# Optimization experiments

Measured on AMD Instinct MI355X. Metric: run time of the kernel, lower is better.

## Reference

```python
import jax, jax.numpy as jnp
import numpy as np

B, S, D = 2, 4096, 512   # batch, seq_len, input_dim
W, H = 256, 4            # memory width (d_model), attention heads
DH = W // H              # per-head depth


def _dense(x, w, b):
    return x @ w + b


def setup_inputs() -> dict:
    key = jax.random.key(0)
    ks = jax.random.split(key, 24)
    def w(k, shape):
        return jax.random.normal(k, shape, dtype=jnp.float32) * 0.02
    inp = {
        "x": jax.random.normal(ks[0], (B, S, D), dtype=jnp.float32),
        # outer q/k/v projections D -> W
        "qp_w": w(ks[1], (D, W)), "qp_b": jnp.zeros((W,), jnp.float32),
        "kp_w": w(ks[2], (D, W)), "kp_b": jnp.zeros((W,), jnp.float32),
        "vp_w": w(ks[3], (D, W)), "vp_b": jnp.zeros((W,), jnp.float32),
        # MHA internal projections W -> W
        "wq_w": w(ks[4], (W, W)), "wq_b": jnp.zeros((W,), jnp.float32),
        "wk_w": w(ks[5], (W, W)), "wk_b": jnp.zeros((W,), jnp.float32),
        "wv_w": w(ks[6], (W, W)), "wv_b": jnp.zeros((W,), jnp.float32),
        "wo_w": w(ks[7], (W, W)), "wo_b": jnp.zeros((W,), jnp.float32),
        # deep MLP memory (depth=2, gelu) + its output proj W -> W
        "m0_w": w(ks[8], (W, W)), "m0_b": jnp.zeros((W,), jnp.float32),
        "m1_w": w(ks[9], (W, W)), "m1_b": jnp.zeros((W,), jnp.float32),
        "mo_w": w(ks[10], (W, W)), "mo_b": jnp.zeros((W,), jnp.float32),
        # final output projection W -> D
        "op_w": w(ks[11], (W, D)), "op_b": jnp.zeros((D,), jnp.float32),
    }
    return inp


def reference(x, qp_w, qp_b, kp_w, kp_b, vp_w, vp_b,
              wq_w, wq_b, wk_w, wk_b, wv_w, wv_b, wo_w, wo_b,
              m0_w, m0_b, m1_w, m1_b, mo_w, mo_b, op_w, op_b):
    # outer projections (D -> W)
    q0 = _dense(x, qp_w, qp_b)
    k0 = _dense(x, kp_w, kp_b)
    v0 = _dense(x, vp_w, vp_b)
    # MHA internal projections (W -> W)
    q = _dense(q0, wq_w, wq_b)
    k = _dense(k0, wk_w, wk_b)
    v = _dense(v0, wv_w, wv_b)
    # split heads: [B,S,W] -> [B,H,S,DH]
    def split(t):
        return t.reshape(B, S, H, DH).transpose(0, 2, 1, 3)
    qh, kh, vh = split(q), split(k), split(v)
    scores = jnp.einsum('bhqd,bhkd->bhqk', qh, kh) / jnp.sqrt(jnp.float32(DH))
    attn = jax.nn.softmax(scores, axis=-1)
    ctx = jnp.einsum('bhqk,bhkd->bhqd', attn, vh)
    ctx = ctx.transpose(0, 2, 1, 3).reshape(B, S, W)
    retrieved = _dense(ctx, wo_w, wo_b)
    # deep MLP memory (exact gelu, matching keras 'gelu')
    h = jax.nn.gelu(_dense(retrieved, m0_w, m0_b), approximate=False)
    h = jax.nn.gelu(_dense(h, m1_w, m1_b), approximate=False)
    mem = _dense(h, mo_w, mo_b)
    # final projection + residual
    out = _dense(mem, op_w, op_b) + x
    return out
```

## Files before the change

### kernel.cpp

```cpp
#include <hip/hip_runtime.h>
#include <cstdint>
#include <cstddef>


#define GAS(p) ((const __attribute__((address_space(1))) void*)(p))
#define LAS(p) ((__attribute__((address_space(3))) void*)(p))

typedef __attribute__((ext_vector_type(8))) short bfrag;
typedef __attribute__((ext_vector_type(4))) float facc;
typedef uint16_t u16;

__device__ __forceinline__ u16 f2bf(float f) {
  uint32_t u = __float_as_uint(f);
  u += 0x7fffu + ((u >> 16) & 1u);
  return (u16)(u >> 16);
}
__device__ __forceinline__ float bf2f(u16 h) {
  return __uint_as_float((uint32_t)h << 16);
}
__device__ __forceinline__ float gelu_exact(float v) {
  return 0.5f * v * (1.f + erff(v * 0.70710678118654752440f));
}
__device__ __forceinline__ facc mfma16(bfrag a, bfrag b, facc c) {
  return __builtin_amdgcn_mfma_f32_16x16x32_bf16(a, b, c, 0, 0, 0);
}

__device__ __forceinline__ bfrag lds_frag(const u16* lds, int row, int kk, int ln) {
  int kb  = (kk << 6) + ((ln >> 4) << 4);
  int off = (row << 7) + (kb ^ ((row & 7) << 4));
  return *(const bfrag*)((const char*)lds + off);
}

template <int ROWS>
__device__ __forceinline__ void stage_tile(const u16* gbase, int ldK, u16* lds,
                                           int wv, int ln) {
#pragma unroll
  for (int i = 0; i < ROWS / 32; i++) {
    int seg = (i << 2) + wv;
    int row = (seg << 3) + (ln >> 3);
    int kb  = (ln & 7) << 4;
    const char* g = (const char*)(gbase + (size_t)row * ldK) +
                    (kb ^ ((row & 7) << 4));
    __builtin_amdgcn_global_load_lds(GAS(g), LAS(lds + (seg << 9)), 16, 0, 0);
  }
}

template <int EPI, int BN>
__global__ __launch_bounds__(256) void gemm_bt(
    const u16* __restrict__ A, const u16* __restrict__ Bt,
    const float* __restrict__ bias, const float* __restrict__ resid,
    u16* __restrict__ obf, float* __restrict__ of32,
    u16* __restrict__ qb, u16* __restrict__ kb2, u16* __restrict__ vb,
    int M, int N, int K, int zsA, int zsB, int zRows) {
  const int t = threadIdx.x, wv = t >> 6, ln = t & 63;
  const int wr = wv >> 1, wc = wv & 1;
  const int m0 = blockIdx.y << 7, n0 = blockIdx.x * BN;
  const int z = blockIdx.z;
  A  += (size_t)z * zsA;
  Bt += (size_t)z * zsB;
  constexpr int NJ = BN / 32;

  __shared__ __align__(16) u16 Al[128 * 64];
  __shared__ __align__(16) u16 Bl[BN * 64];

  facc acc[4][NJ];
#pragma unroll
  for (int i = 0; i < 4; i++)
#pragma unroll
    for (int j = 0; j < NJ; j++)
#pragma unroll
      for (int r = 0; r < 4; r++) acc[i][j][r] = 0.f;

  const u16* Ab = A + (size_t)m0 * K;
  const u16* Bb = Bt + (size_t)n0 * K;
  stage_tile<128>(Ab, K, Al, wv, ln);
  stage_tile<BN>(Bb, K, Bl, wv, ln);

  const int nk = K >> 6;
  for (int kt = 0; kt < nk; ++kt) {
    __syncthreads();
#pragma unroll
    for (int kk = 0; kk < 2; kk++) {
      bfrag av[4], bv[NJ];
#pragma unroll
      for (int i = 0; i < 4; i++)
        av[i] = lds_frag(Al, (wr << 6) + (i << 4) + (ln & 15), kk, ln);
#pragma unroll
      for (int j = 0; j < NJ; j++)
        bv[j] = lds_frag(Bl, wc * (BN / 2) + (j << 4) + (ln & 15), kk, ln);
#pragma unroll
      for (int i = 0; i < 4; i++)
#pragma unroll
        for (int j = 0; j < NJ; j++)
          acc[i][j] = mfma16(av[i], bv[j], acc[i][j]);
    }
    if (kt + 1 < nk) {
      __syncthreads();
      stage_tile<128>(Ab + (kt + 1) * 64, K, Al, wv, ln);
      stage_tile<BN>(Bb + (kt + 1) * 64, K, Bl, wv, ln);
    }
  }

  const int rb = (ln >> 4) << 2, cb = ln & 15;
#pragma unroll
  for (int i = 0; i < 4; i++) {
#pragma unroll
    for (int j = 0; j < NJ; j++) {
      const int col = n0 + wc * (BN / 2) + (j << 4) + cb;
      const float bcol = bias ? bias[col] : 0.f;
#pragma unroll
      for (int r = 0; r < 4; r++) {
        const int row = m0 + (wr << 6) + (i << 4) + rb + r;
        float val = acc[i][j][r] + bcol;
        if (EPI == 0) {
          obf[(size_t)(z * zRows + row) * N + col] = f2bf(val);
        } else if (EPI == 1) {
          obf[(size_t)row * N + col] = f2bf(gelu_exact(val));
        } else if (EPI == 2) {
          const int sec = col >> 8, cc = col & 255, h = cc >> 6, dh = cc & 63;
          const int b = row >> 12, s = row & 4095;
          const size_t idx = (((size_t)(b * 4 + h)) * 4096 + s) * 64 + dh;
          const u16 bvv = f2bf(val);
          if (sec == 0) qb[idx] = bvv;
          else if (sec == 1) kb2[idx] = bvv;
          else vb[idx] = bvv;
        } else {
          of32[(size_t)row * N + col] = val + resid[(size_t)row * N + col];
        }
      }
    }
  }
}

__global__ __launch_bounds__(256) void attn2(
    const u16* __restrict__ qg, const u16* __restrict__ kg,
    const u16* __restrict__ vtg, u16* __restrict__ Opart,
    float* __restrict__ lpart) {
  const int t = threadIdx.x, wv = t >> 6, ln = t & 63;
  const int lo = ln & 15, hi = ln >> 4;
  const int qt = blockIdx.x, bh = blockIdx.y, half = blockIdx.z;
  const int qbase = qt * 128 + wv * 32;
  const u16* Q  = qg + ((size_t)bh * 4096 + qbase) * 64;
  const u16* Kb = kg + ((size_t)bh * 4096 + half * 2048) * 64;
  const u16* Vt = vtg + (size_t)bh * 64 * 4096 + half * 2048;

  __shared__ __align__(16) u16 Klds[2][4096];
  __shared__ __align__(16) u16 Vlds[2][4096];
  __shared__ __align__(16) u16 Plds[4][2048];
  u16* Pw = Plds[wv];

  bfrag qf[2][2];
#pragma unroll
  for (int g = 0; g < 2; g++) {
    const u16* qp = Q + (((g << 4) + lo) << 6) + (hi << 3);
    qf[g][0] = *(const bfrag*)qp;
    qf[g][1] = *(const bfrag*)(qp + 32);
  }
  facc oacc[2][4];
#pragma unroll
  for (int g = 0; g < 2; g++)
#pragma unroll
    for (int nb = 0; nb < 4; nb++)
#pragma unroll
      for (int r = 0; r < 4; r++) oacc[g][nb][r] = 0.f;
  float l_acc[2] = {0.f, 0.f};

  stage_tile<64>(Kb, 64, Klds[0], wv, ln);
  stage_tile<64>(Vt, 4096, Vlds[0], wv, ln);

  for (int kt = 0; kt < 32; ++kt) {
    const int cur = kt & 1;
    __syncthreads();
    if (kt < 31) {
      stage_tile<64>(Kb + (size_t)(kt + 1) * 64 * 64, 64, Klds[cur ^ 1], wv, ln);
      stage_tile<64>(Vt + (kt + 1) * 64, 4096, Vlds[cur ^ 1], wv, ln);
    }
    facc sa[2][4];
#pragma unroll
    for (int g = 0; g < 2; g++)
#pragma unroll
      for (int kb = 0; kb < 4; kb++)
#pragma unroll
        for (int r = 0; r < 4; r++) sa[g][kb][r] = 0.f;
#pragma unroll
    for (int kb = 0; kb < 4; kb++) {
      bfrag a0 = lds_frag(Klds[cur], (kb << 4) + lo, 0, ln);
      bfrag a1 = lds_frag(Klds[cur], (kb << 4) + lo, 1, ln);
      sa[0][kb] = mfma16(a0, qf[0][0], sa[0][kb]);
      sa[0][kb] = mfma16(a1, qf[0][1], sa[0][kb]);
      sa[1][kb] = mfma16(a0, qf[1][0], sa[1][kb]);
      sa[1][kb] = mfma16(a1, qf[1][1], sa[1][kb]);
    }
#pragma unroll
    for (int g = 0; g < 2; g++) {
      const int row = (g << 4) + lo;
      char* pb = (char*)Pw + (row << 7);
      const int sw = (row & 7) << 4;
      float ls = 0.f;
#pragma unroll
      for (int kb = 0; kb < 4; kb++) {
        float p0 = exp2f(sa[g][kb][0] * 0.18033688011112042f);
        float p1 = exp2f(sa[g][kb][1] * 0.18033688011112042f);
        float p2 = exp2f(sa[g][kb][2] * 0.18033688011112042f);
        float p3 = exp2f(sa[g][kb][3] * 0.18033688011112042f);
        ls += (p0 + p1) + (p2 + p3);
        uint32_t w0, w1;
        asm("v_cvt_pk_bf16_f32 %0, %1, %2" : "=v"(w0) : "v"(p0), "v"(p1));
        asm("v_cvt_pk_bf16_f32 %0, %1, %2" : "=v"(w1) : "v"(p2), "v"(p3));
        uint2 w2;
        w2.x = w0; w2.y = w1;
        *(uint2*)(pb + (((kb << 5) + (hi << 3)) ^ sw)) = w2;
      }
      l_acc[g] += ls;
    }
#pragma unroll
    for (int c = 0; c < 2; c++) {
      bfrag pa0 = lds_frag(Pw, lo, c, ln);
      bfrag pa1 = lds_frag(Pw, 16 + lo, c, ln);
#pragma unroll
      for (int nb = 0; nb < 4; nb++) {
        bfrag vf = lds_frag(Vlds[cur], (nb << 4) + lo, c, ln);
        oacc[0][nb] = mfma16(pa0, vf, oacc[0][nb]);
        oacc[1][nb] = mfma16(pa1, vf, oacc[1][nb]);
      }
    }
  }

#pragma unroll
  for (int g = 0; g < 2; g++) {
    l_acc[g] += __shfl_xor(l_acc[g], 16);
    l_acc[g] += __shfl_xor(l_acc[g], 32);
  }
  const size_t obase = (size_t)(half * 8 + bh) * 4096;
#pragma unroll
  for (int g = 0; g < 2; g++) {
#pragma unroll
    for (int nb = 0; nb < 4; nb++)
#pragma unroll
      for (int r = 0; r < 4; r++) {
        const int q = qbase + (g << 4) + (hi << 2) + r;
        Opart[(obase + q) * 64 + (nb << 4) + lo] = f2bf(oacc[g][nb][r]);
      }
    if (hi == 0) lpart[obase + qbase + (g << 4) + lo] = l_acc[g];
  }
}

__global__ __launch_bounds__(256) void attn_combine(
    const u16* __restrict__ Opart, const float* __restrict__ lpart,
    u16* __restrict__ ctx) {
  const int idx = blockIdx.x * 256 + threadIdx.x;
  const int d0 = (idx & 7) << 3, s = (idx >> 3) & 4095, bh = idx >> 15;
  const size_t o0 = ((size_t)bh * 4096 + s) * 64 + d0;
  const size_t o1 = o0 + (size_t)8 * 4096 * 64;
  bfrag a = *(const bfrag*)(Opart + o0);
  bfrag b = *(const bfrag*)(Opart + o1);
  const float rl = 1.f / (lpart[bh * 4096 + s] + lpart[32768 + bh * 4096 + s]);
  bfrag o;
#pragma unroll
  for (int j = 0; j < 8; j++)
    o[j] = (short)f2bf((bf2f((u16)a[j]) + bf2f((u16)b[j])) * rl);
  *(bfrag*)(ctx + ((size_t)(bh >> 2) * 4096 + s) * 256 + ((bh & 3) << 6) + d0) = o;
}

__global__ __launch_bounds__(256) void conv_bf16(const float* __restrict__ x,
                                                 u16* __restrict__ xb) {
  const size_t i = ((size_t)blockIdx.x * 256 + threadIdx.x) * 8;
  float4 a = *(const float4*)(x + i);
  float4 b = *(const float4*)(x + i + 4);
  bfrag o;
  o[0] = (short)f2bf(a.x); o[1] = (short)f2bf(a.y);
  o[2] = (short)f2bf(a.z); o[3] = (short)f2bf(a.w);
  o[4] = (short)f2bf(b.x); o[5] = (short)f2bf(b.y);
  o[6] = (short)f2bf(b.z); o[7] = (short)f2bf(b.w);
  *(bfrag*)(xb + i) = o;
}

__global__ __launch_bounds__(256) void conv_weights(
    const float* __restrict__ qp, const float* __restrict__ kp,
    const float* __restrict__ vp, const float* __restrict__ mo,
    u16* __restrict__ owqkv, u16* __restrict__ mo_bf) {
  const int i = (blockIdx.x * 256 + threadIdx.x) * 4;
  const float* s; u16* dst; int off;
  if (i < 131072)      { s = qp; dst = owqkv;          off = i; }
  else if (i < 262144) { s = kp; dst = owqkv + 131072; off = i - 131072; }
  else if (i < 393216) { s = vp; dst = owqkv + 262144; off = i - 262144; }
  else                 { s = mo; dst = mo_bf;          off = i - 393216; }
  float4 v = *(const float4*)(s + off);
  ushort4 o;
  o.x = f2bf(v.x); o.y = f2bf(v.y); o.z = f2bf(v.z); o.w = f2bf(v.w);
  *(ushort4*)(dst + off) = o;
}

__global__ __launch_bounds__(256) void transp_w6(
    const float* wo, const float* m0, const float* m1,
    const float* wq, const float* wk, const float* wv,
    u16* wo_t, u16* m0_t, u16* m1_t, u16* wqT, u16* wkT, u16* wvT) {
  const int mi = blockIdx.x >> 8, n = blockIdx.x & 255, k = threadIdx.x;
  const float* s; u16* d;
  switch (mi) {
    case 0: s = wo; d = wo_t; break;
    case 1: s = m0; d = m0_t; break;
    case 2: s = m1; d = m1_t; break;
    case 3: s = wq; d = wqT; break;
    case 4: s = wk; d = wkT; break;
    default: s = wv; d = wvT; break;
  }
  d[(size_t)n * 256 + k] = f2bf(s[(size_t)k * 256 + n]);
}

__global__ __launch_bounds__(256) void transp_op(const float* __restrict__ op_w,
                                                 u16* __restrict__ opT) {
  const int d = blockIdx.x, c = threadIdx.x;
  opT[(size_t)d * 256 + c] = f2bf(op_w[(size_t)c * 512 + d]);
}

__global__ __launch_bounds__(256) void fuse_bias(
    const float* qp_b, const float* kp_b, const float* vp_b,
    const float* wq_w, const float* wk_w, const float* wv_w,
    const float* wq_b, const float* wk_b, const float* wv_b,
    const float* mo_b, const float* op_w, const float* op_b,
    float* bqkv, float* bmo) {
  const int z = blockIdx.x, t = threadIdx.x;
  __shared__ float red[4];
  float v;
  if (z < 768) {
    const int sec = z >> 8, nn = z & 255;
    const float* ob = sec == 0 ? qp_b : (sec == 1 ? kp_b : vp_b);
    const float* iw = sec == 0 ? wq_w : (sec == 1 ? wk_w : wv_w);
    v = ob[t] * iw[(size_t)t * 256 + nn];
  } else {
    v = mo_b[t] * op_w[(size_t)t * 512 + (z - 768)];
  }
#pragma unroll
  for (int o = 32; o > 0; o >>= 1) v += __shfl_down(v, o);
  if ((t & 63) == 0) red[t >> 6] = v;
  __syncthreads();
  if (t == 0) {
    float s = red[0] + red[1] + red[2] + red[3];
    if (z < 768) {
      const int sec = z >> 8, nn = z & 255;
      const float* ib = sec == 0 ? wq_b : (sec == 1 ? wk_b : wv_b);
      bqkv[z] = s + ib[nn];
    } else {
      bmo[z - 768] = s + op_b[z - 768];
    }
  }
}

__global__ __launch_bounds__(256) void transpose_v(const u16* __restrict__ v,
                                                   u16* __restrict__ vt) {
  const int bh = blockIdx.x >> 6, st = blockIdx.x & 63, t = threadIdx.x;
  __shared__ u16 tile[64][65];
  const u16* src = v + ((size_t)bh * 4096 + st * 64) * 64;
  {
    const int r = t >> 2, c0 = (t & 3) << 4;
    bfrag x0 = *(const bfrag*)(src + (size_t)r * 64 + c0);
    bfrag x1 = *(const bfrag*)(src + (size_t)r * 64 + c0 + 8);
#pragma unroll
    for (int j = 0; j < 8; j++) {
      tile[r][c0 + j] = (u16)x0[j];
      tile[r][c0 + 8 + j] = (u16)x1[j];
    }
  }
  __syncthreads();
  {
    const int d = t >> 2, s0 = (t & 3) << 4;
    bfrag y0, y1;
#pragma unroll
    for (int j = 0; j < 8; j++) {
      y0[j] = (short)tile[s0 + j][d];
      y1[j] = (short)tile[s0 + 8 + j][d];
    }
    u16* dst = vt + ((size_t)bh * 64 + d) * 4096 + (st << 6) + s0;
    *(bfrag*)(dst) = y0;
    *(bfrag*)(dst + 8) = y1;
  }
}

extern "C" void kernel_launch(void* const* d_in, const int* in_sizes, int n_in,
                              void* d_out, int out_size, void* d_ws,
                              size_t ws_size, hipStream_t stream) {
  const float* x    = (const float*)d_in[0];
  const float* qp_w = (const float*)d_in[1];
  const float* qp_b = (const float*)d_in[2];
  const float* kp_w = (const float*)d_in[3];
  const float* kp_b = (const float*)d_in[4];
  const float* vp_w = (const float*)d_in[5];
  const float* vp_b = (const float*)d_in[6];
  const float* wq_w = (const float*)d_in[7];
  const float* wq_b = (const float*)d_in[8];
  const float* wk_w = (const float*)d_in[9];
  const float* wk_b = (const float*)d_in[10];
  const float* wv_w = (const float*)d_in[11];
  const float* wv_b = (const float*)d_in[12];
  const float* wo_w = (const float*)d_in[13];
  const float* wo_b = (const float*)d_in[14];
  const float* m0_w = (const float*)d_in[15];
  const float* m0_b = (const float*)d_in[16];
  const float* m1_w = (const float*)d_in[17];
  const float* m1_b = (const float*)d_in[18];
  const float* mo_w = (const float*)d_in[19];
  const float* mo_b = (const float*)d_in[20];
  const float* op_w = (const float*)d_in[21];
  const float* op_b = (const float*)d_in[22];
  float* out = (float*)d_out;

  char* ws = (char*)d_ws;
  u16*   xb     = (u16*)(ws);
  u16*   q_buf  = (u16*)(ws + 8388608);
  u16*   k_buf  = (u16*)(ws + 12582912);
  u16*   v_buf  = (u16*)(ws + 16777216);
  u16*   vt_buf = (u16*)(ws + 20971520);
  u16*   ctx    = (u16*)(ws + 25165824);
  u16*   Opart  = (u16*)(ws + 29360128);
  float* lpart  = (float*)(ws + 37748736);
  u16*   Wqkv_t = (u16*)(ws + 38010880);
  u16*   owqkv  = (u16*)(ws + 38797312);
  u16*   wqkvT  = (u16*)(ws + 39583744);
  u16*   wo_t   = (u16*)(ws + 39976960);
  u16*   m0_t   = (u16*)(ws + 40108032);
  u16*   m1_t   = (u16*)(ws + 40239104);
  u16*   opT    = (u16*)(ws + 40370176);
  u16*   mo_bf  = (u16*)(ws + 40632320);
  u16*   Wmo_t  = (u16*)(ws + 40763392);
  float* bqkv   = (float*)(ws + 41025536);
  float* bmo    = (float*)(ws + 41029632);
  u16* retr = v_buf;
  u16* h1   = q_buf;
  u16* h2   = k_buf;

  conv_bf16<<<2048, 256, 0, stream>>>(x, xb);
  conv_weights<<<448, 256, 0, stream>>>(qp_w, kp_w, vp_w, m0_w ? mo_w : mo_w,
                                        owqkv, mo_bf);
  transp_w6<<<1536, 256, 0, stream>>>(wo_w, m0_w, m1_w, wq_w, wk_w, wv_w,
                                      wo_t, m0_t, m1_t,
                                      wqkvT, wqkvT + 65536, wqkvT + 131072);
  transp_op<<<512, 256, 0, stream>>>(op_w, opT);
  fuse_bias<<<1280, 256, 0, stream>>>(qp_b, kp_b, vp_b, wq_w, wk_w, wv_w,
                                      wq_b, wk_b, wv_b, mo_b, op_w, op_b,
                                      bqkv, bmo);
  gemm_bt<0, 128><<<dim3(4, 2, 3), 256, 0, stream>>>(
      wqkvT, owqkv, nullptr, nullptr, Wqkv_t, nullptr, nullptr, nullptr,
      nullptr, 256, 512, 256, 256 * 256, 512 * 256, 256);
  gemm_bt<0, 64><<<dim3(4, 4), 256, 0, stream>>>(
      opT, mo_bf, nullptr, nullptr, Wmo_t, nullptr, nullptr, nullptr,
      nullptr, 512, 256, 256, 0, 0, 0);

  gemm_bt<2, 128><<<dim3(6, 64), 256, 0, stream>>>(
      xb, Wqkv_t, bqkv, nullptr, nullptr, nullptr, q_buf, k_buf, v_buf,
      8192, 768, 512, 0, 0, 0);
  transpose_v<<<512, 256, 0, stream>>>(v_buf, vt_buf);
  attn2<<<dim3(32, 8, 2), 256, 0, stream>>>(q_buf, k_buf, vt_buf, Opart, lpart);
  attn_combine<<<1024, 256, 0, stream>>>(Opart, lpart, ctx);

  gemm_bt<0, 64><<<dim3(4, 64), 256, 0, stream>>>(
      ctx, wo_t, wo_b, nullptr, retr, nullptr, nullptr, nullptr, nullptr,
      8192, 256, 256, 0, 0, 0);
  gemm_bt<1, 64><<<dim3(4, 64), 256, 0, stream>>>(
      retr, m0_t, m0_b, nullptr, h1, nullptr, nullptr, nullptr, nullptr,
      8192, 256, 256, 0, 0, 0);
  gemm_bt<1, 64><<<dim3(4, 64), 256, 0, stream>>>(
      h1, m1_t, m1_b, nullptr, h2, nullptr, nullptr, nullptr, nullptr,
      8192, 256, 256, 0, 0, 0);
  gemm_bt<3, 128><<<dim3(4, 64), 256, 0, stream>>>(
      h2, Wmo_t, bmo, x, nullptr, out, nullptr, nullptr, nullptr,
      8192, 512, 256, 0, 0, 0);
}
```

Baseline: 272.1 us.

## Rewrite attention with 32x32 MFMA in registers, fold wo into m0, merge prep kernels

The attention kernel now uses 32x32x16 bf16 MFMAs and keeps P in registers via permlane32 swaps instead of an LDS round trip. Row sums come from an MFMA against a ones vector, and the softmax scale is folded into Q in the QKV epilogue. KV is split four ways with a 4-way combine, and wo_w is algebraically merged with m0_w so one 8192x256 GEMM disappears. The weight conversion and transpose launches are consolidated into fewer kernels. Softmax still skips max subtraction as before, and the extra bf16 rounding of the fused weight may change accuracy slightly.

```diff
diff --git a/kernel.cpp b/kernel.cpp
--- a/kernel.cpp
+++ b/kernel.cpp
@@ -8,6 +8,7 @@
 
 typedef __attribute__((ext_vector_type(8))) short bfrag;
 typedef __attribute__((ext_vector_type(4))) float facc;
+typedef __attribute__((ext_vector_type(16))) float facc16;
 typedef uint16_t u16;
 
 __device__ __forceinline__ u16 f2bf(float f) {
@@ -24,10 +25,19 @@
 __device__ __forceinline__ facc mfma16(bfrag a, bfrag b, facc c) {
   return __builtin_amdgcn_mfma_f32_16x16x32_bf16(a, b, c, 0, 0, 0);
 }
+__device__ __forceinline__ facc16 mfma32(bfrag a, bfrag b, facc16 c) {
+  return __builtin_amdgcn_mfma_f32_32x32x16_bf16(a, b, c, 0, 0, 0);
+}
+
+union U4 { uint32_t w[4]; bfrag f; };
 
 __device__ __forceinline__ bfrag lds_frag(const u16* lds, int row, int kk, int ln) {
   int kb  = (kk << 6) + ((ln >> 4) << 4);
   int off = (row << 7) + (kb ^ ((row & 7) << 4));
+  return *(const bfrag*)((const char*)lds + off);
+}
+__device__ __forceinline__ bfrag lds_frag_rb(const u16* lds, int row, int bytecol) {
+  int off = (row << 7) + (bytecol ^ ((row & 7) << 4));
   return *(const bfrag*)((const char*)lds + off);
 }
 
@@ -120,10 +130,9 @@
           const int sec = col >> 8, cc = col & 255, h = cc >> 6, dh = cc & 63;
           const int b = row >> 12, s = row & 4095;
           const size_t idx = (((size_t)(b * 4 + h)) * 4096 + s) * 64 + dh;
-          const u16 bvv = f2bf(val);
-          if (sec == 0) qb[idx] = bvv;
-          else if (sec == 1) kb2[idx] = bvv;
-          else vb[idx] = bvv;
+          if (sec == 0) qb[idx] = f2bf(val * 0.18033688011112042f);
+          else if (sec == 1) kb2[idx] = f2bf(val);
+          else vb[idx] = f2bf(val);
         } else {
           of32[(size_t)row * N + col] = val + resid[(size_t)row * N + col];
         }
@@ -132,194 +141,203 @@
   }
 }
 
-__global__ __launch_bounds__(256) void attn2(
+__global__ __launch_bounds__(256) void attn3(
     const u16* __restrict__ qg, const u16* __restrict__ kg,
     const u16* __restrict__ vtg, u16* __restrict__ Opart,
     float* __restrict__ lpart) {
   const int t = threadIdx.x, wv = t >> 6, ln = t & 63;
-  const int lo = ln & 15, hi = ln >> 4;
-  const int qt = blockIdx.x, bh = blockIdx.y, half = blockIdx.z;
-  const int qbase = qt * 128 + wv * 32;
+  const int l31 = ln & 31, lh = ln >> 5;
+  const int qt = blockIdx.x, bh = blockIdx.y, kv = blockIdx.z;
+  const int qbase = qt * 256 + wv * 64;
   const u16* Q  = qg + ((size_t)bh * 4096 + qbase) * 64;
-  const u16* Kb = kg + ((size_t)bh * 4096 + half * 2048) * 64;
-  const u16* Vt = vtg + (size_t)bh * 64 * 4096 + half * 2048;
+  const u16* Kb = kg + ((size_t)bh * 4096 + kv * 1024) * 64;
+  const u16* Vt = vtg + (size_t)bh * 64 * 4096 + kv * 1024;
 
   __shared__ __align__(16) u16 Klds[2][4096];
   __shared__ __align__(16) u16 Vlds[2][4096];
-  __shared__ __align__(16) u16 Plds[4][2048];
-  u16* Pw = Plds[wv];
-
-  bfrag qf[2][2];
-#pragma unroll
-  for (int g = 0; g < 2; g++) {
-    const u16* qp = Q + (((g << 4) + lo) << 6) + (hi << 3);
-    qf[g][0] = *(const bfrag*)qp;
-    qf[g][1] = *(const bfrag*)(qp + 32);
-  }
-  facc oacc[2][4];
-#pragma unroll
-  for (int g = 0; g < 2; g++)
-#pragma unroll
-    for (int nb = 0; nb < 4; nb++)
-#pragma unroll
-      for (int r = 0; r < 4; r++) oacc[g][nb][r] = 0.f;
-  float l_acc[2] = {0.f, 0.f};
+
+  bfrag qf[2][4];
+#pragma unroll
+  for (int qi = 0; qi < 2; qi++) {
+    const u16* qp = Q + (size_t)(((qi << 5) + l31) << 6) + (lh << 3);
+#pragma unroll
+    for (int dc = 0; dc < 4; dc++)
+      qf[qi][dc] = *(const bfrag*)(qp + (dc << 4));
+  }
+  bfrag ones;
+#pragma unroll
+  for (int j = 0; j < 8; j++) ones[j] = (short)0x3F80;
+
+  facc16 oacc[2][2];
+  facc16 lacc[2];
+#pragma unroll
+  for (int qi = 0; qi < 2; qi++) {
+#pragma unroll
+    for (int r = 0; r < 16; r++) {
+      oacc[qi][0][r] = 0.f; oacc[qi][1][r] = 0.f; lacc[qi][r] = 0.f;
+    }
+  }
 
   stage_tile<64>(Kb, 64, Klds[0], wv, ln);
   stage_tile<64>(Vt, 4096, Vlds[0], wv, ln);
 
-  for (int kt = 0; kt < 32; ++kt) {
+  for (int kt = 0; kt < 16; ++kt) {
     const int cur = kt & 1;
     __syncthreads();
-    if (kt < 31) {
+    if (kt < 15) {
       stage_tile<64>(Kb + (size_t)(kt + 1) * 64 * 64, 64, Klds[cur ^ 1], wv, ln);
       stage_tile<64>(Vt + (kt + 1) * 64, 4096, Vlds[cur ^ 1], wv, ln);
     }
-    facc sa[2][4];
-#pragma unroll
-    for (int g = 0; g < 2; g++)
-#pragma unroll
-      for (int kb = 0; kb < 4; kb++)
-#pragma unroll
-        for (int r = 0; r < 4; r++) sa[g][kb][r] = 0.f;
-#pragma unroll
-    for (int kb = 0; kb < 4; kb++) {
-      bfrag a0 = lds_frag(Klds[cur], (kb << 4) + lo, 0, ln);
-      bfrag a1 = lds_frag(Klds[cur], (kb << 4) + lo, 1, ln);
-      sa[0][kb] = mfma16(a0, qf[0][0], sa[0][kb]);
-      sa[0][kb] = mfma16(a1, qf[0][1], sa[0][kb]);
-      sa[1][kb] = mfma16(a0, qf[1][0], sa[1][kb]);
-      sa[1][kb] = mfma16(a1, qf[1][1], sa[1][kb]);
-    }
-#pragma unroll
-    for (int g = 0; g < 2; g++) {
-      const int row = (g << 4) + lo;
-      char* pb = (char*)Pw + (row << 7);
-      const int sw = (row & 7) << 4;
-      float ls = 0.f;
-#pragma unroll
-      for (int kb = 0; kb < 4; kb++) {
-        float p0 = exp2f(sa[g][kb][0] * 0.18033688011112042f);
-        float p1 = exp2f(sa[g][kb][1] * 0.18033688011112042f);
-        float p2 = exp2f(sa[g][kb][2] * 0.18033688011112042f);
-        float p3 = exp2f(sa[g][kb][3] * 0.18033688011112042f);
-        ls += (p0 + p1) + (p2 + p3);
-        uint32_t w0, w1;
-        asm("v_cvt_pk_bf16_f32 %0, %1, %2" : "=v"(w0) : "v"(p0), "v"(p1));
-        asm("v_cvt_pk_bf16_f32 %0, %1, %2" : "=v"(w1) : "v"(p2), "v"(p3));
-        uint2 w2;
-        w2.x = w0; w2.y = w1;
-        *(uint2*)(pb + (((kb << 5) + (hi << 3)) ^ sw)) = w2;
+#pragma unroll
+    for (int kb = 0; kb < 2; kb++) {
+      bfrag kf[4];
+#pragma unroll
+      for (int dc = 0; dc < 4; dc++)
+        kf[dc] = lds_frag_rb(Klds[cur], (kb << 5) + l31, (dc << 5) + (lh << 4));
+
+      bfrag pa[2][2];
+#pragma unroll
+      for (int qi = 0; qi < 2; qi++) {
+        facc16 sa;
+#pragma unroll
+        for (int r = 0; r < 16; r++) sa[r] = 0.f;
+#pragma unroll
+        for (int dc = 0; dc < 4; dc++)
+          sa = mfma32(kf[dc], qf[qi][dc], sa);
+        float p[16];
+#pragma unroll
+        for (int r = 0; r < 16; r++) p[r] = exp2f(sa[r]);
+        uint32_t u0, u1, u2, u3, u4, u5, u6, u7;
+        asm("v_cvt_pk_bf16_f32 %0, %1, %2" : "=v"(u0) : "v"(p[0]),  "v"(p[1]));
+        asm("v_cvt_pk_bf16_f32 %0, %1, %2" : "=v"(u1) : "v"(p[2]),  "v"(p[3]));
+        asm("v_cvt_pk_bf16_f32 %0, %1, %2" : "=v"(u2) : "v"(p[4]),  "v"(p[5]));
+        asm("v_cvt_pk_bf16_f32 %0, %1, %2" : "=v"(u3) : "v"(p[6]),  "v"(p[7]));
+        asm("v_cvt_pk_bf16_f32 %0, %1, %2" : "=v"(u4) : "v"(p[8]),  "v"(p[9]));
+        asm("v_cvt_pk_bf16_f32 %0, %1, %2" : "=v"(u5) : "v"(p[10]), "v"(p[11]));
+        asm("v_cvt_pk_bf16_f32 %0, %1, %2" : "=v"(u6) : "v"(p[12]), "v"(p[13]));
+        asm("v_cvt_pk_bf16_f32 %0, %1, %2" : "=v"(u7) : "v"(p[14]), "v"(p[15]));
+        asm volatile("v_permlane32_swap_b32 %0, %1" : "+v"(u0), "+v"(u2));
+        asm volatile("v_permlane32_swap_b32 %0, %1" : "+v"(u1), "+v"(u3));
+        asm volatile("v_permlane32_swap_b32 %0, %1" : "+v"(u4), "+v"(u6));
+        asm volatile("v_permlane32_swap_b32 %0, %1" : "+v"(u5), "+v"(u7));
+        U4 c0; c0.w[0] = u0; c0.w[1] = u1; c0.w[2] = u2; c0.w[3] = u3;
+        U4 c1; c1.w[0] = u4; c1.w[1] = u5; c1.w[2] = u6; c1.w[3] = u7;
+        pa[qi][0] = c0.f;
+        pa[qi][1] = c1.f;
       }
-      l_acc[g] += ls;
-    }
-#pragma unroll
-    for (int c = 0; c < 2; c++) {
-      bfrag pa0 = lds_frag(Pw, lo, c, ln);
-      bfrag pa1 = lds_frag(Pw, 16 + lo, c, ln);
-#pragma unroll
-      for (int nb = 0; nb < 4; nb++) {
-        bfrag vf = lds_frag(Vlds[cur], (nb << 4) + lo, c, ln);
-        oacc[0][nb] = mfma16(pa0, vf, oacc[0][nb]);
-        oacc[1][nb] = mfma16(pa1, vf, oacc[1][nb]);
+#pragma unroll
+      for (int c = 0; c < 2; c++) {
+#pragma unroll
+        for (int dj = 0; dj < 2; dj++) {
+          bfrag vf = lds_frag_rb(Vlds[cur], (dj << 5) + l31,
+                                 (kb << 6) + (c << 5) + (lh << 4));
+          oacc[0][dj] = mfma32(pa[0][c], vf, oacc[0][dj]);
+          oacc[1][dj] = mfma32(pa[1][c], vf, oacc[1][dj]);
+        }
+        lacc[0] = mfma32(pa[0][c], ones, lacc[0]);
+        lacc[1] = mfma32(pa[1][c], ones, lacc[1]);
       }
     }
   }
 
-#pragma unroll
-  for (int g = 0; g < 2; g++) {
-    l_acc[g] += __shfl_xor(l_acc[g], 16);
-    l_acc[g] += __shfl_xor(l_acc[g], 32);
-  }
-  const size_t obase = (size_t)(half * 8 + bh) * 4096;
-#pragma unroll
-  for (int g = 0; g < 2; g++) {
-#pragma unroll
-    for (int nb = 0; nb < 4; nb++)
-#pragma unroll
-      for (int r = 0; r < 4; r++) {
-        const int q = qbase + (g << 4) + (hi << 2) + r;
-        Opart[(obase + q) * 64 + (nb << 4) + lo] = f2bf(oacc[g][nb][r]);
-      }
-    if (hi == 0) lpart[obase + qbase + (g << 4) + lo] = l_acc[g];
-  }
-}
-
-__global__ __launch_bounds__(256) void attn_combine(
+  const size_t obase = (size_t)(kv * 8 + bh) * 4096 + qbase;
+#pragma unroll
+  for (int qi = 0; qi < 2; qi++) {
+#pragma unroll
+    for (int r = 0; r < 16; r++) {
+      const int qrow = (qi << 5) + (r & 3) + ((r >> 2) << 3) + (lh << 2);
+#pragma unroll
+      for (int dj = 0; dj < 2; dj++)
+        Opart[(obase + qrow) * 64 + (dj << 5) + l31] = f2bf(oacc[qi][dj][r]);
+      if (l31 == 0) lpart[obase + qrow] = lacc[qi][r];
+    }
+  }
+}
+
+__global__ __launch_bounds__(256) void attn_combine4(
     const u16* __restrict__ Opart, const float* __restrict__ lpart,
     u16* __restrict__ ctx) {
   const int idx = blockIdx.x * 256 + threadIdx.x;
   const int d0 = (idx & 7) << 3, s = (idx >> 3) & 4095, bh = idx >> 15;
-  const size_t o0 = ((size_t)bh * 4096 + s) * 64 + d0;
-  const size_t o1 = o0 + (size_t)8 * 4096 * 64;
-  bfrag a = *(const bfrag*)(Opart + o0);
-  bfrag b = *(const bfrag*)(Opart + o1);
-  const float rl = 1.f / (lpart[bh * 4096 + s] + lpart[32768 + bh * 4096 + s]);
+  const size_t sb = (size_t)bh * 4096 + s;
+  float acc[8] = {0.f, 0.f, 0.f, 0.f, 0.f, 0.f, 0.f, 0.f};
+  float lsum = 0.f;
+#pragma unroll
+  for (int pz = 0; pz < 4; pz++) {
+    const size_t pb = (size_t)pz * 8 * 4096;
+    bfrag a = *(const bfrag*)(Opart + (pb + sb) * 64 + d0);
+#pragma unroll
+    for (int j = 0; j < 8; j++) acc[j] += bf2f((u16)a[j]);
+    lsum += lpart[pb + sb];
+  }
+  const float rl = 1.f / lsum;
   bfrag o;
 #pragma unroll
-  for (int j = 0; j < 8; j++)
-    o[j] = (short)f2bf((bf2f((u16)a[j]) + bf2f((u16)b[j])) * rl);
+  for (int j = 0; j < 8; j++) o[j] = (short)f2bf(acc[j] * rl);
   *(bfrag*)(ctx + ((size_t)(bh >> 2) * 4096 + s) * 256 + ((bh & 3) << 6) + d0) = o;
 }
 
-__global__ __launch_bounds__(256) void conv_bf16(const float* __restrict__ x,
-                                                 u16* __restrict__ xb) {
-  const size_t i = ((size_t)blockIdx.x * 256 + threadIdx.x) * 8;
-  float4 a = *(const float4*)(x + i);
-  float4 b = *(const float4*)(x + i + 4);
-  bfrag o;
-  o[0] = (short)f2bf(a.x); o[1] = (short)f2bf(a.y);
-  o[2] = (short)f2bf(a.z); o[3] = (short)f2bf(a.w);
-  o[4] = (short)f2bf(b.x); o[5] = (short)f2bf(b.y);
-  o[6] = (short)f2bf(b.z); o[7] = (short)f2bf(b.w);
-  *(bfrag*)(xb + i) = o;
-}
-
-__global__ __launch_bounds__(256) void conv_weights(
-    const float* __restrict__ qp, const float* __restrict__ kp,
-    const float* __restrict__ vp, const float* __restrict__ mo,
-    u16* __restrict__ owqkv, u16* __restrict__ mo_bf) {
-  const int i = (blockIdx.x * 256 + threadIdx.x) * 4;
-  const float* s; u16* dst; int off;
-  if (i < 131072)      { s = qp; dst = owqkv;          off = i; }
-  else if (i < 262144) { s = kp; dst = owqkv + 131072; off = i - 131072; }
-  else if (i < 393216) { s = vp; dst = owqkv + 262144; off = i - 262144; }
-  else                 { s = mo; dst = mo_bf;          off = i - 393216; }
-  float4 v = *(const float4*)(s + off);
-  ushort4 o;
-  o.x = f2bf(v.x); o.y = f2bf(v.y); o.z = f2bf(v.z); o.w = f2bf(v.w);
-  *(ushort4*)(dst + off) = o;
-}
-
-__global__ __launch_bounds__(256) void transp_w6(
-    const float* wo, const float* m0, const float* m1,
+__global__ __launch_bounds__(256) void conv_all(
+    const float* __restrict__ x, const float* __restrict__ qp,
+    const float* __restrict__ kp, const float* __restrict__ vp,
+    const float* __restrict__ mo, const float* __restrict__ wo,
+    u16* __restrict__ xb, u16* __restrict__ owqkv,
+    u16* __restrict__ mo_bf, u16* __restrict__ wo_bf) {
+  const int bid = blockIdx.x;
+  if (bid < 2048) {
+    const size_t i = ((size_t)bid * 256 + threadIdx.x) * 8;
+    float4 a = *(const float4*)(x + i);
+    float4 b = *(const float4*)(x + i + 4);
+    bfrag o;
+    o[0] = (short)f2bf(a.x); o[1] = (short)f2bf(a.y);
+    o[2] = (short)f2bf(a.z); o[3] = (short)f2bf(a.w);
+    o[4] = (short)f2bf(b.x); o[5] = (short)f2bf(b.y);
+    o[6] = (short)f2bf(b.z); o[7] = (short)f2bf(b.w);
+    *(bfrag*)(xb + i) = o;
+  } else {
+    const int i = ((bid - 2048) * 256 + threadIdx.x) * 4;
+    const float* s; u16* dst; int off;
+    if (i < 131072)      { s = qp; dst = owqkv;          off = i; }
+    else if (i < 262144) { s = kp; dst = owqkv + 131072; off = i - 131072; }
+    else if (i < 393216) { s = vp; dst = owqkv + 262144; off = i - 262144; }
+    else if (i < 458752) { s = mo; dst = mo_bf;          off = i - 393216; }
+    else                 { s = wo; dst = wo_bf;          off = i - 458752; }
+    float4 v = *(const float4*)(s + off);
+    ushort4 o;
+    o.x = f2bf(v.x); o.y = f2bf(v.y); o.z = f2bf(v.z); o.w = f2bf(v.w);
+    *(ushort4*)(dst + off) = o;
+  }
+}
+
+__global__ __launch_bounds__(256) void transp_all(
     const float* wq, const float* wk, const float* wv,
-    u16* wo_t, u16* m0_t, u16* m1_t, u16* wqT, u16* wkT, u16* wvT) {
-  const int mi = blockIdx.x >> 8, n = blockIdx.x & 255, k = threadIdx.x;
-  const float* s; u16* d;
-  switch (mi) {
-    case 0: s = wo; d = wo_t; break;
-    case 1: s = m0; d = m0_t; break;
-    case 2: s = m1; d = m1_t; break;
-    case 3: s = wq; d = wqT; break;
-    case 4: s = wk; d = wkT; break;
-    default: s = wv; d = wvT; break;
-  }
-  d[(size_t)n * 256 + k] = f2bf(s[(size_t)k * 256 + n]);
-}
-
-__global__ __launch_bounds__(256) void transp_op(const float* __restrict__ op_w,
-                                                 u16* __restrict__ opT) {
-  const int d = blockIdx.x, c = threadIdx.x;
-  opT[(size_t)d * 256 + c] = f2bf(op_w[(size_t)c * 512 + d]);
-}
-
-__global__ __launch_bounds__(256) void fuse_bias(
+    const float* m0, const float* m1, const float* op_w,
+    u16* wqkvT, u16* m0_t, u16* m1_t, u16* opT) {
+  const int bid = blockIdx.x;
+  if (bid < 1280) {
+    const int mi = bid >> 8, n = bid & 255, k = threadIdx.x;
+    const float* s; u16* d;
+    switch (mi) {
+      case 0: s = wq; d = wqkvT; break;
+      case 1: s = wk; d = wqkvT + 65536; break;
+      case 2: s = wv; d = wqkvT + 131072; break;
+      case 3: s = m0; d = m0_t; break;
+      default: s = m1; d = m1_t; break;
+    }
+    d[(size_t)n * 256 + k] = f2bf(s[(size_t)k * 256 + n]);
+  } else {
+    const int d = bid - 1280, c = threadIdx.x;
+    opT[(size_t)d * 256 + c] = f2bf(op_w[(size_t)c * 512 + d]);
+  }
+}
+
+__global__ __launch_bounds__(256) void fuse_bias3(
     const float* qp_b, const float* kp_b, const float* vp_b,
     const float* wq_w, const float* wk_w, const float* wv_w,
     const float* wq_b, const float* wk_b, const float* wv_b,
     const float* mo_b, const float* op_w, const float* op_b,
-    float* bqkv, float* bmo) {
+    const float* wo_b, const float* m0_w, const float* m0_b,
+    float* bqkv, float* bmo, float* bf1) {
   const int z = blockIdx.x, t = threadIdx.x;
   __shared__ float red[4];
   float v;
@@ -328,8 +346,10 @@
     const float* ob = sec == 0 ? qp_b : (sec == 1 ? kp_b : vp_b);
     const float* iw = sec == 0 ? wq_w : (sec == 1 ? wk_w : wv_w);
     v = ob[t] * iw[(size_t)t * 256 + nn];
+  } else if (z < 1280) {
+    v = mo_b[t] * op_w[(size_t)t * 512 + (z - 768)];
   } else {
-    v = mo_b[t] * op_w[(size_t)t * 512 + (z - 768)];
+    v = wo_b[t] * m0_w[(size_t)t * 256 + (z - 1280)];
   }
 #pragma unroll
   for (int o = 32; o > 0; o >>= 1) v += __shfl_down(v, o);
@@ -341,8 +361,10 @@
       const int sec = z >> 8, nn = z & 255;
       const float* ib = sec == 0 ? wq_b : (sec == 1 ? wk_b : wv_b);
       bqkv[z] = s + ib[nn];
+    } else if (z < 1280) {
+      bmo[z - 768] = s + op_b[z - 768];
     } else {
-      bmo[z - 768] = s + op_b[z - 768];
+      bf1[z - 1280] = s + m0_b[z - 1280];
     }
   }
 }
@@ -407,41 +429,42 @@
 
   char* ws = (char*)d_ws;
   u16*   xb     = (u16*)(ws);
-  u16*   q_buf  = (u16*)(ws + 8388608);
-  u16*   k_buf  = (u16*)(ws + 12582912);
-  u16*   v_buf  = (u16*)(ws + 16777216);
-  u16*   vt_buf = (u16*)(ws + 20971520);
-  u16*   ctx    = (u16*)(ws + 25165824);
-  u16*   Opart  = (u16*)(ws + 29360128);
-  float* lpart  = (float*)(ws + 37748736);
-  u16*   Wqkv_t = (u16*)(ws + 38010880);
-  u16*   owqkv  = (u16*)(ws + 38797312);
-  u16*   wqkvT  = (u16*)(ws + 39583744);
-  u16*   wo_t   = (u16*)(ws + 39976960);
-  u16*   m0_t   = (u16*)(ws + 40108032);
-  u16*   m1_t   = (u16*)(ws + 40239104);
-  u16*   opT    = (u16*)(ws + 40370176);
-  u16*   mo_bf  = (u16*)(ws + 40632320);
-  u16*   Wmo_t  = (u16*)(ws + 40763392);
-  float* bqkv   = (float*)(ws + 41025536);
-  float* bmo    = (float*)(ws + 41029632);
-  u16* retr = v_buf;
-  u16* h1   = q_buf;
-  u16* h2   = k_buf;
-
-  conv_bf16<<<2048, 256, 0, stream>>>(x, xb);
-  conv_weights<<<448, 256, 0, stream>>>(qp_w, kp_w, vp_w, m0_w ? mo_w : mo_w,
-                                        owqkv, mo_bf);
-  transp_w6<<<1536, 256, 0, stream>>>(wo_w, m0_w, m1_w, wq_w, wk_w, wv_w,
-                                      wo_t, m0_t, m1_t,
-                                      wqkvT, wqkvT + 65536, wqkvT + 131072);
-  transp_op<<<512, 256, 0, stream>>>(op_w, opT);
-  fuse_bias<<<1280, 256, 0, stream>>>(qp_b, kp_b, vp_b, wq_w, wk_w, wv_w,
-                                      wq_b, wk_b, wv_b, mo_b, op_w, op_b,
-                                      bqkv, bmo);
+  u16*   v_buf  = (u16*)(ws + 8388608);
+  u16*   Opart  = (u16*)(ws);
+  u16*   q_buf  = (u16*)(ws + 16777216);
+  u16*   k_buf  = (u16*)(ws + 20971520);
+  u16*   vt_buf = (u16*)(ws + 25165824);
+  u16*   ctx    = (u16*)(ws + 29360128);
+  float* lpart  = (float*)(ws + 33554432);
+  u16*   owqkv  = (u16*)(ws + 34078720);
+  u16*   wqkvT  = (u16*)(ws + 34865152);
+  u16*   Wqkv_t = (u16*)(ws + 35258368);
+  u16*   m0_t   = (u16*)(ws + 36044800);
+  u16*   m1_t   = (u16*)(ws + 36175872);
+  u16*   opT    = (u16*)(ws + 36306944);
+  u16*   mo_bf  = (u16*)(ws + 36569088);
+  u16*   wo_bf  = (u16*)(ws + 36700160);
+  u16*   Wf1_t  = (u16*)(ws + 36831232);
+  u16*   Wmo_t  = (u16*)(ws + 36962304);
+  float* bqkv   = (float*)(ws + 37224448);
+  float* bmo    = (float*)(ws + 37227520);
+  float* bf1    = (float*)(ws + 37229568);
+  u16* h1 = q_buf;
+  u16* h2 = k_buf;
+
+  conv_all<<<2560, 256, 0, stream>>>(x, qp_w, kp_w, vp_w, mo_w, wo_w,
+                                     xb, owqkv, mo_bf, wo_bf);
+  transp_all<<<1792, 256, 0, stream>>>(wq_w, wk_w, wv_w, m0_w, m1_w, op_w,
+                                       wqkvT, m0_t, m1_t, opT);
+  fuse_bias3<<<1536, 256, 0, stream>>>(qp_b, kp_b, vp_b, wq_w, wk_w, wv_w,
+                                       wq_b, wk_b, wv_b, mo_b, op_w, op_b,
+                                       wo_b, m0_w, m0_b, bqkv, bmo, bf1);
   gemm_bt<0, 128><<<dim3(4, 2, 3), 256, 0, stream>>>(
       wqkvT, owqkv, nullptr, nullptr, Wqkv_t, nullptr, nullptr, nullptr,
-      nullptr, 256, 512, 256, 256 * 256, 512 * 256, 256);
+      nullptr, 256, 512, 256, 65536, 131072, 256);
+  gemm_bt<0, 64><<<dim3(4, 2), 256, 0, stream>>>(
+      m0_t, wo_bf, nullptr, nullptr, Wf1_t, nullptr, nullptr, nullptr,
+      nullptr, 256, 256, 256, 0, 0, 0);
   gemm_bt<0, 64><<<dim3(4, 4), 256, 0, stream>>>(
       opT, mo_bf, nullptr, nullptr, Wmo_t, nullptr, nullptr, nullptr,
       nullptr, 512, 256, 256, 0, 0, 0);
@@ -450,14 +473,11 @@
       xb, Wqkv_t, bqkv, nullptr, nullptr, nullptr, q_buf, k_buf, v_buf,
       8192, 768, 512, 0, 0, 0);
   transpose_v<<<512, 256, 0, stream>>>(v_buf, vt_buf);
-  attn2<<<dim3(32, 8, 2), 256, 0, stream>>>(q_buf, k_buf, vt_buf, Opart, lpart);
-  attn_combine<<<1024, 256, 0, stream>>>(Opart, lpart, ctx);
-
-  gemm_bt<0, 64><<<dim3(4, 64), 256, 0, stream>>>(
-      ctx, wo_t, wo_b, nullptr, retr, nullptr, nullptr, nullptr, nullptr,
-      8192, 256, 256, 0, 0, 0);
+  attn3<<<dim3(16, 8, 4), 256, 0, stream>>>(q_buf, k_buf, vt_buf, Opart, lpart);
+  attn_combine4<<<1024, 256, 0, stream>>>(Opart, lpart, ctx);
+
   gemm_bt<1, 64><<<dim3(4, 64), 256, 0, stream>>>(
-      retr, m0_t, m0_b, nullptr, h1, nullptr, nullptr, nullptr, nullptr,
+      ctx, Wf1_t, bf1, nullptr, h1, nullptr, nullptr, nullptr, nullptr,
       8192, 256, 256, 0, 0, 0);
   gemm_bt<1, 64><<<dim3(4, 64), 256, 0, stream>>>(
       h1, m1_t, m1_b, nullptr, h2, nullptr, nullptr, nullptr, nullptr,
```

After: 271.5 us. Within noise of the previous version (-0.2%).
